# Performance work log

Hardware: AMD Instinct MI355X
Metric: run time of the kernel (lower is better)

## Reference

```python
import math
import jax, jax.numpy as jnp
import numpy as np

B, S, D_MODEL = 4, 2048, 512
H, D_KV = 8, 64
NUM_BUCKETS = 32
MAX_DISTANCE = 128  # T5 default


def _relative_position_bucket(rel_pos, bidirectional=True, num_buckets=NUM_BUCKETS, max_distance=MAX_DISTANCE):
    # Standard T5 bucketing (encoder: bidirectional=True since is_decoder=False).
    ret = jnp.zeros_like(rel_pos)
    if bidirectional:
        num_buckets //= 2
        ret = (rel_pos > 0).astype(jnp.int32) * num_buckets
        rel_pos = jnp.abs(rel_pos)
    else:
        rel_pos = -jnp.minimum(rel_pos, 0)
    max_exact = num_buckets // 2
    is_small = rel_pos < max_exact
    safe_rp = jnp.maximum(rel_pos, 1)  # avoid log(0); masked out by is_small
    val_if_large = max_exact + (
        jnp.log(safe_rp.astype(jnp.float32) / max_exact)
        / math.log(max_distance / max_exact)
        * (num_buckets - max_exact)
    ).astype(jnp.int32)
    val_if_large = jnp.minimum(val_if_large, num_buckets - 1)
    return ret + jnp.where(is_small, rel_pos, val_if_large)


def setup_inputs() -> dict:
    key = jax.random.key(0)
    ks = jax.random.split(key, 8)
    query = jax.random.normal(ks[0], (B, S, D_MODEL), dtype=jnp.float32)
    kk = jax.random.normal(ks[1], (B, S, D_MODEL), dtype=jnp.float32)
    vv = jax.random.normal(ks[2], (B, S, D_MODEL), dtype=jnp.float32)
    key_mask = jnp.ones((B, S), dtype=jnp.float32)
    scale = 1.0 / math.sqrt(D_MODEL)
    Wq = jax.random.normal(ks[3], (D_MODEL, H * D_KV), dtype=jnp.float32) * scale
    Wk = jax.random.normal(ks[4], (D_MODEL, H * D_KV), dtype=jnp.float32) * scale
    Wv = jax.random.normal(ks[5], (D_MODEL, H * D_KV), dtype=jnp.float32) * scale
    rel_emb = jax.random.normal(ks[6], (NUM_BUCKETS, H), dtype=jnp.float32) * 0.1
    return {"query": query, "key": kk, "value": vv, "key_mask": key_mask,
            "Wq": Wq, "Wk": Wk, "Wv": Wv, "rel_emb": rel_emb, "start_pos": 0}


def reference(query, key, value, key_mask, Wq, Wk, Wv, rel_emb, start_pos):
    Bq, Q, _ = query.shape
    K = key.shape[1]
    # projections (training path: no cache; equals start_pos=0 prefill)
    q = (query @ Wq).reshape(Bq, Q, H, D_KV)  # [B,Q,H,d]
    k = (key @ Wk).reshape(Bq, K, H, D_KV)
    v = (value @ Wv).reshape(Bq, K, H, D_KV)
    # T5: no 1/sqrt(d) scaling
    scores = jnp.einsum("bqhd,bkhd->bhqk", q, k)  # [B,H,Q,K]
    # relative position bias over [K,K], sliced to last Q rows
    ctx = jnp.arange(K)[:, None]
    mem = jnp.arange(K)[None, :]
    buckets = _relative_position_bucket(mem - ctx)  # [K,K]
    bias = rel_emb[buckets]  # [K,K,H]
    bias = jnp.transpose(bias, (2, 0, 1))[None, :, -Q:, :]  # [1,H,Q,K]
    scores = scores + bias
    # additive key mask
    add_mask = (1.0 - key_mask)[:, None, None, :] * -10000.0
    scores = scores + add_mask
    probs = jax.nn.softmax(scores, axis=-1)
    context = jnp.einsum("bhqk,bkhd->bqhd", probs, v)
    return context.reshape(Bq, Q, H * D_KV)
```

## Files before the change

kernel.cpp:

```cpp
#include <hip/hip_runtime.h>
#include <hip/hip_bf16.h>

typedef __attribute__((ext_vector_type(8))) _Float16 half8;
typedef __attribute__((ext_vector_type(2))) __fp16 fp16x2;
typedef __attribute__((ext_vector_type(4))) float f32x4;

#define LOG2E 1.4426950408889634f

__global__ __launch_bounds__(256) void cvt_h_kernel(const float* __restrict__ q,
                                                    const float* __restrict__ k,
                                                    const float* __restrict__ v,
                                                    _Float16* __restrict__ xq,
                                                    _Float16* __restrict__ xk,
                                                    _Float16* __restrict__ xv) {
  const int z = blockIdx.y;
  const float* x = z == 0 ? q : z == 1 ? k : v;
  _Float16* y = z == 0 ? xq : z == 1 ? xk : xv;
  size_t i = (size_t)blockIdx.x * 256 + threadIdx.x;
  const f32x4* p = (const f32x4*)x + i * 2;
  f32x4 a = p[0], b = p[1];
  half8 o;
  o[0] = (_Float16)a[0]; o[1] = (_Float16)a[1];
  o[2] = (_Float16)a[2]; o[3] = (_Float16)a[3];
  o[4] = (_Float16)b[0]; o[5] = (_Float16)b[1];
  o[6] = (_Float16)b[2]; o[7] = (_Float16)b[3];
  ((half8*)y)[i] = o;
}

__global__ __launch_bounds__(256) void wtrans_kernel(const float* __restrict__ Wq,
                                                     const float* __restrict__ Wk,
                                                     const float* __restrict__ Wv,
                                                     _Float16* __restrict__ wtq,
                                                     _Float16* __restrict__ wtk,
                                                     _Float16* __restrict__ wtv) {
  const int z = blockIdx.z;
  const float* W = z == 0 ? Wq : z == 1 ? Wk : Wv;
  _Float16* Wt = z == 0 ? wtq : z == 1 ? wtk : wtv;
  __shared__ float tile[32][33];
  int k0 = blockIdx.x * 32, n0 = blockIdx.y * 32;
  int c = threadIdx.x & 31, r0 = threadIdx.x >> 5;
  #pragma unroll
  for (int rr = 0; rr < 32; rr += 8)
    tile[r0 + rr][c] = W[(size_t)(k0 + r0 + rr) * 512 + n0 + c];
  __syncthreads();
  #pragma unroll
  for (int rr = 0; rr < 32; rr += 8)
    Wt[(size_t)(n0 + r0 + rr) * 512 + k0 + c] = (_Float16)tile[c][r0 + rr];
}

__global__ __launch_bounds__(256) void proj_kernel(const _Float16* __restrict__ Xq,
                                                   const _Float16* __restrict__ Xk,
                                                   const _Float16* __restrict__ Xv,
                                                   const _Float16* __restrict__ Wtq,
                                                   const _Float16* __restrict__ Wtk,
                                                   const _Float16* __restrict__ Wtv,
                                                   _Float16* __restrict__ Qp,
                                                   _Float16* __restrict__ Kp,
                                                   _Float16* __restrict__ Vt) {
  const int z = blockIdx.z;
  const _Float16* X  = z == 0 ? Xq : z == 1 ? Xk : Xv;
  const _Float16* Wt = z == 0 ? Wtq : z == 1 ? Wtk : Wtv;
  _Float16* outp     = z == 0 ? Qp : z == 1 ? Kp : Vt;

  __shared__ __align__(16) char lt_all[4 * 64 * 144];
  const int wave = threadIdx.x >> 6, lane = threadIdx.x & 63;
  const int g = lane >> 4, li = lane & 15;
  const int m0 = blockIdx.x * 128 + wave * 32;
  const int h = blockIdx.y;

  f32x4 acc[2][4];
  #pragma unroll
  for (int i = 0; i < 2; ++i)
    #pragma unroll
    for (int j = 0; j < 4; ++j) acc[i][j] = (f32x4){0.f, 0.f, 0.f, 0.f};

  const _Float16* xa = X + (size_t)m0 * 512;
  const _Float16* wb = Wt + (size_t)(h << 6) * 512;

  for (int k0 = 0; k0 < 512; k0 += 32) {
    half8 a[2], bw[4];
    #pragma unroll
    for (int rt = 0; rt < 2; ++rt)
      a[rt] = *(const half8*)(xa + (size_t)(rt * 16 + li) * 512 + k0 + g * 8);
    #pragma unroll
    for (int ct = 0; ct < 4; ++ct)
      bw[ct] = *(const half8*)(wb + (size_t)(ct * 16 + li) * 512 + k0 + g * 8);
    #pragma unroll
    for (int rt = 0; rt < 2; ++rt)
      #pragma unroll
      for (int ct = 0; ct < 4; ++ct)
        acc[rt][ct] = __builtin_amdgcn_mfma_f32_16x16x32_f16(a[rt], bw[ct], acc[rt][ct], 0, 0, 0);
  }

  const float qs = (z == 0) ? LOG2E : 1.0f;
  const int bidx = m0 >> 11, sbase = m0 & 2047;
  if (z != 2) {
    #pragma unroll
    for (int rt = 0; rt < 2; ++rt)
      #pragma unroll
      for (int r = 0; r < 4; ++r) {
        int s = sbase + rt * 16 + g * 4 + r;
        _Float16* orow = outp + ((size_t)((bidx * 8 + h) * 2048 + s) << 6);
        #pragma unroll
        for (int ct = 0; ct < 4; ++ct)
          orow[ct * 16 + li] = (_Float16)(acc[rt][ct][r] * qs);
      }
  } else {
    char* lt = lt_all + wave * (64 * 144);
    #pragma unroll
    for (int rt = 0; rt < 2; ++rt)
      #pragma unroll
      for (int ct = 0; ct < 4; ++ct)
        #pragma unroll
        for (int r = 0; r < 4; ++r) {
          int d = ct * 16 + li, sl = rt * 16 + g * 4 + r;
          *(_Float16*)(lt + d * 144 + ((sl * 2) ^ ((d & 7) << 4))) = (_Float16)acc[rt][ct][r];
        }
    __syncthreads();
    int d = lane;
    _Float16* vrow = outp + (size_t)((bidx * 8 + h) * 64 + d) * 2048 + sbase;
    #pragma unroll
    for (int c = 0; c < 4; ++c) {
      half8 vv = *(half8*)(lt + d * 144 + ((c * 16) ^ ((d & 7) << 4)));
      *(half8*)(vrow + c * 8) = vv;
    }
  }
}

__global__ __launch_bounds__(64, 2) void attn_kernel(const _Float16* __restrict__ Qp,
                                                     const _Float16* __restrict__ Kp,
                                                     const _Float16* __restrict__ Vt,
                                                     const float* __restrict__ kmask,
                                                     const float* __restrict__ rel_emb,
                                                     float* __restrict__ outp) {
  __shared__ float bias_tab[256];
  __shared__ __align__(16) char pb[2 * 2048];
  const int fid = blockIdx.x;
  const int nid = (fid & 7) * 256 + (fid >> 3);
  const int qt = nid & 63, bh = nid >> 6;
  const int b = bh >> 3, h = bh & 7;
  const int lane = threadIdx.x;
  const int g = lane >> 4, li = lane & 15;
  const int qw = qt * 32;

  for (int idx = lane; idx < 256; idx += 64) {
    int rel = idx - 128;
    int ret = rel > 0 ? 16 : 0;
    int rp = rel < 0 ? -rel : rel;
    int bb;
    if (rp < 8) bb = rp;
    else {
      int t = (rp >= 12) + (rp >= 16) + (rp >= 23) + (rp >= 32) +
              (rp >= 46) + (rp >= 64) + (rp >= 91);
      bb = 8 + t;
    }
    bias_tab[idx] = rel_emb[(ret + bb) * 8 + h] * LOG2E;
  }
  const float far_neg = rel_emb[15 * 8 + h] * LOG2E;
  const float far_pos = rel_emb[31 * 8 + h] * LOG2E;
  const float MASKC = 10000.0f * LOG2E;

  const _Float16* Qb = Qp + (size_t)bh * (2048 * 64);
  const _Float16* Kb = Kp + (size_t)bh * (2048 * 64);
  const _Float16* Vb = Vt + (size_t)bh * (64 * 2048);
  const float* mkb = kmask + b * 2048;

  half8 qa[2][2];
  #pragma unroll
  for (int s = 0; s < 2; ++s)
    #pragma unroll
    for (int kc = 0; kc < 2; ++kc)
      qa[s][kc] = *(const half8*)(Qb + (size_t)(qw + s * 16 + li) * 64 + kc * 32 + g * 8);

  f32x4 o[2][4];
  float m[2], l[2];
  #pragma unroll
  for (int s = 0; s < 2; ++s) {
    #pragma unroll
    for (int ct = 0; ct < 4; ++ct) o[s][ct] = (f32x4){0.f, 0.f, 0.f, 0.f};
    m[s] = -1e30f; l[s] = 0.f;
  }

  const int swz = (li & 7) << 4;
  half8 kA[4][2], kB[4][2];

  #pragma unroll
  for (int jt = 0; jt < 4; ++jt)
    #pragma unroll
    for (int kc = 0; kc < 2; ++kc)
      kA[jt][kc] = *(const half8*)(Kb + (size_t)(jt * 16 + li) * 64 + kc * 32 + g * 8);

  __syncthreads();

#define PREFETCH(DST, JN)                                                        \
  {                                                                              \
    int jn_ = (JN) < 2048 ? (JN) : 0;                                            \
    _Pragma("unroll")                                                            \
    for (int jt = 0; jt < 4; ++jt)                                               \
      _Pragma("unroll")                                                          \
      for (int kc = 0; kc < 2; ++kc)                                             \
        DST[jt][kc] = *(const half8*)(Kb + (size_t)(jn_ + jt * 16 + li) * 64 +   \
                                      kc * 32 + g * 8);                          \
  }

#define PROCESS(KB, J0)                                                          \
  {                                                                              \
    const int jb = (J0);            \
    f32x4 sc[2][4];                                                              \
    _Pragma("unroll")                                                            \
    for (int s = 0; s < 2; ++s)                                                  \
      _Pragma("unroll")                                                          \
      for (int jt = 0; jt < 4; ++jt) {                                           \
        f32x4 zz = (f32x4){0.f, 0.f, 0.f, 0.f};                                  \
        zz = __builtin_amdgcn_mfma_f32_16x16x32_f16(KB[jt][0], qa[s][0], zz, 0, 0, 0); \
        sc[s][jt] = __builtin_amdgcn_mfma_f32_16x16x32_f16(KB[jt][1], qa[s][1], zz, 0, 0, 0); \
      }                                                                          \
    _Pragma("unroll")                                                            \
    for (int jt = 0; jt < 4; ++jt) {                                             \
      int jlo = jb + jt * 16;                                                    \
      f32x4 m4 = *(const f32x4*)(mkb + jlo + 4 * g);                             \
      _Pragma("unroll")                                                          \
      for (int s = 0; s < 2; ++s) {                                              \
        int qlo = qw + s * 16;                                                   \
        if (jlo - (qlo + 15) >= 91) {                                            \
          _Pragma("unroll")                                                      \
          for (int r = 0; r < 4; ++r)                                            \
            sc[s][jt][r] += far_pos + (m4[r] - 1.0f) * MASKC;                    \
        } else if (jlo + 15 - qlo <= -91) {                                      \
          _Pragma("unroll")                                                      \
          for (int r = 0; r < 4; ++r)                                            \
            sc[s][jt][r] += far_neg + (m4[r] - 1.0f) * MASKC;                    \
        } else {                                                                 \
          int base = jlo + 4 * g - qlo - li + 128;                               \
          _Pragma("unroll")                                                      \
          for (int r = 0; r < 4; ++r)                                            \
            sc[s][jt][r] += bias_tab[base + r] + (m4[r] - 1.0f) * MASKC;         \
        }                                                                        \
      }                                                                          \
    }                                                                            \
    _Pragma("unroll")                                                            \
    for (int s = 0; s < 2; ++s) {                                                \
      float t = sc[s][0][0];                                                     \
      _Pragma("unroll")                                                          \
      for (int jt = 0; jt < 4; ++jt)                                             \
        _Pragma("unroll")                                                        \
        for (int r = 0; r < 4; ++r) t = fmaxf(t, sc[s][jt][r]);                  \
      t = fmaxf(t, __shfl_xor(t, 16));                                           \
      t = fmaxf(t, __shfl_xor(t, 32));                                           \
      float mnew = fmaxf(m[s], t);                                               \
      float scal = exp2f(m[s] - mnew);                                           \
      m[s] = mnew;                                                               \
      l[s] *= scal;                                                              \
      _Pragma("unroll")                                                          \
      for (int ct = 0; ct < 4; ++ct) o[s][ct] *= scal;                           \
      _Pragma("unroll")                                                          \
      for (int jt = 0; jt < 4; ++jt) {                                           \
        float p0 = exp2f(sc[s][jt][0] - m[s]), p1 = exp2f(sc[s][jt][1] - m[s]);  \
        float p2 = exp2f(sc[s][jt][2] - m[s]), p3 = exp2f(sc[s][jt][3] - m[s]);  \
        l[s] += (p0 + p1) + (p2 + p3);                                           \
        fp16x2 h01 = __builtin_amdgcn_cvt_pkrtz(p0, p1);                         \
        fp16x2 h23 = __builtin_amdgcn_cvt_pkrtz(p2, p3);                         \
        uint2 w;                                                                 \
        w.x = __builtin_bit_cast(unsigned, h01);                                 \
        w.y = __builtin_bit_cast(unsigned, h23);                                 \
        *(uint2*)(pb + s * 2048 + li * 128 + ((32 * jt + 8 * g) ^ swz)) = w;     \
      }                                                                          \
    }                                                                            \
    half8 pa[2][2];                                                              \
    _Pragma("unroll")                                                            \
    for (int s = 0; s < 2; ++s) {                                                \
      pa[s][0] = *(half8*)(pb + s * 2048 + li * 128 + ((16 * g) ^ swz));         \
      pa[s][1] = *(half8*)(pb + s * 2048 + li * 128 + ((64 + 16 * g) ^ swz));    \
    }                                                                            \
    __builtin_amdgcn_s_setprio(1);                                               \
    _Pragma("unroll")                                                            \
    for (int dct = 0; dct < 4; ++dct) {                                          \
      half8 vb0 = *(const half8*)(Vb + (size_t)(dct * 16 + li) * 2048 + jb + g * 8);      \
      half8 vb1 = *(const half8*)(Vb + (size_t)(dct * 16 + li) * 2048 + jb + 32 + g * 8); \
      _Pragma("unroll")                                                          \
      for (int s = 0; s < 2; ++s) {                                              \
        o[s][dct] = __builtin_amdgcn_mfma_f32_16x16x32_f16(vb0, pa[s][0], o[s][dct], 0, 0, 0); \
        o[s][dct] = __builtin_amdgcn_mfma_f32_16x16x32_f16(vb1, pa[s][1], o[s][dct], 0, 0, 0); \
      }                                                                          \
    }                                                                            \
    __builtin_amdgcn_s_setprio(0);                                               \
  }

  for (int j0 = 0; j0 < 2048; j0 += 128) {
    PREFETCH(kB, j0 + 64)
    PROCESS(kA, j0)
    PREFETCH(kA, j0 + 128)
    PROCESS(kB, j0 + 64)
  }
#undef PREFETCH
#undef PROCESS

  #pragma unroll
  for (int s = 0; s < 2; ++s) {
    float lf = l[s];
    lf += __shfl_xor(lf, 16);
    lf += __shfl_xor(lf, 32);
    float inv = 1.0f / lf;
    float* orow = outp + ((size_t)b * 2048 + qw + s * 16 + li) * 512 + h * 64;
    #pragma unroll
    for (int dct = 0; dct < 4; ++dct) {
      f32x4 ov = o[s][dct];
      ov[0] *= inv; ov[1] *= inv; ov[2] *= inv; ov[3] *= inv;
      *(f32x4*)(orow + dct * 16 + 4 * g) = ov;
    }
  }
}

extern "C" void kernel_launch(void* const* d_in, const int* in_sizes, int n_in,
                              void* d_out, int out_size, void* d_ws, size_t ws_size,
                              hipStream_t stream) {
  const float* query = (const float*)d_in[0];
  const float* key   = (const float*)d_in[1];
  const float* value = (const float*)d_in[2];
  const float* kmask = (const float*)d_in[3];
  const float* Wq    = (const float*)d_in[4];
  const float* Wk    = (const float*)d_in[5];
  const float* Wv    = (const float*)d_in[6];
  const float* rel   = (const float*)d_in[7];

  char* ws = (char*)d_ws;
  const size_t SZB = 8192ull * 512 * 2;
  const size_t WB  = 512ull * 512 * 2;
  _Float16* xq  = (_Float16*)(ws);
  _Float16* xk  = (_Float16*)(ws + SZB);
  _Float16* xv  = (_Float16*)(ws + 2 * SZB);
  _Float16* wtq = (_Float16*)(ws + 3 * SZB);
  _Float16* wtk = (_Float16*)(ws + 3 * SZB + WB);
  _Float16* wtv = (_Float16*)(ws + 3 * SZB + 2 * WB);
  _Float16* qp  = (_Float16*)(ws + 3 * SZB + 3 * WB);
  _Float16* kp  = (_Float16*)(ws + 4 * SZB + 3 * WB);
  _Float16* vt  = (_Float16*)(ws + 5 * SZB + 3 * WB);

  cvt_h_kernel<<<dim3(2048, 3), dim3(256), 0, stream>>>(query, key, value, xq, xk, xv);
  wtrans_kernel<<<dim3(16, 16, 3), dim3(256), 0, stream>>>(Wq, Wk, Wv, wtq, wtk, wtv);
  proj_kernel<<<dim3(64, 8, 3), dim3(256), 0, stream>>>(xq, xk, xv, wtq, wtk, wtv, qp, kp, vt);
  attn_kernel<<<dim3(2048), dim3(64), 0, stream>>>(qp, kp, vt, kmask, rel, (float*)d_out);
}
```

Before: 326.6 us.

## Split attention key range across two waves with LDS softmax merge

The attention block now uses two waves per 32-query tile. Each wave processes alternating 64-key chunks, and at the end the two partial (max, sum, output) states are merged through shared memory, flash-decoding style. This doubles the waves in flight and halves the serial key loop per wave, aiming to hide latency better. The cost is extra LDS, a barrier and a merge step, and the per-block resource use may limit occupancy. The mask term is also hoisted out of the inner s loop.

```diff
diff --git a/kernel.cpp b/kernel.cpp
--- a/kernel.cpp
+++ b/kernel.cpp
@@ -127,23 +127,24 @@
   }
 }
 
-__global__ __launch_bounds__(64, 2) void attn_kernel(const _Float16* __restrict__ Qp,
-                                                     const _Float16* __restrict__ Kp,
-                                                     const _Float16* __restrict__ Vt,
-                                                     const float* __restrict__ kmask,
-                                                     const float* __restrict__ rel_emb,
-                                                     float* __restrict__ outp) {
+__global__ __launch_bounds__(128, 4) void attn_kernel(const _Float16* __restrict__ Qp,
+                                                      const _Float16* __restrict__ Kp,
+                                                      const _Float16* __restrict__ Vt,
+                                                      const float* __restrict__ kmask,
+                                                      const float* __restrict__ rel_emb,
+                                                      float* __restrict__ outp) {
   __shared__ float bias_tab[256];
-  __shared__ __align__(16) char pb[2 * 2048];
+  __shared__ __align__(16) char pb_all[2 * 4096];
+  __shared__ __align__(16) f32x4 mrg[64][9];
   const int fid = blockIdx.x;
   const int nid = (fid & 7) * 256 + (fid >> 3);
   const int qt = nid & 63, bh = nid >> 6;
   const int b = bh >> 3, h = bh & 7;
-  const int lane = threadIdx.x;
+  const int wave = threadIdx.x >> 6, lane = threadIdx.x & 63;
   const int g = lane >> 4, li = lane & 15;
   const int qw = qt * 32;
 
-  for (int idx = lane; idx < 256; idx += 64) {
+  for (int idx = (int)threadIdx.x; idx < 256; idx += 128) {
     int rel = idx - 128;
     int ret = rel > 0 ? 16 : 0;
     int rp = rel < 0 ? -rel : rel;
@@ -182,13 +183,14 @@
   }
 
   const int swz = (li & 7) << 4;
+  char* pb = pb_all + wave * 4096;
   half8 kA[4][2], kB[4][2];
 
   #pragma unroll
   for (int jt = 0; jt < 4; ++jt)
     #pragma unroll
     for (int kc = 0; kc < 2; ++kc)
-      kA[jt][kc] = *(const half8*)(Kb + (size_t)(jt * 16 + li) * 64 + kc * 32 + g * 8);
+      kA[jt][kc] = *(const half8*)(Kb + (size_t)(wave * 64 + jt * 16 + li) * 64 + kc * 32 + g * 8);
 
   __syncthreads();
 
@@ -219,22 +221,25 @@
     for (int jt = 0; jt < 4; ++jt) {                                             \
       int jlo = jb + jt * 16;                                                    \
       f32x4 m4 = *(const f32x4*)(mkb + jlo + 4 * g);                             \
+      float mt[4];                                                               \
+      _Pragma("unroll")                                                          \
+      for (int r = 0; r < 4; ++r) mt[r] = (m4[r] - 1.0f) * MASKC;                \
       _Pragma("unroll")                                                          \
       for (int s = 0; s < 2; ++s) {                                              \
         int qlo = qw + s * 16;                                                   \
         if (jlo - (qlo + 15) >= 91) {                                            \
           _Pragma("unroll")                                                      \
           for (int r = 0; r < 4; ++r)                                            \
-            sc[s][jt][r] += far_pos + (m4[r] - 1.0f) * MASKC;                    \
+            sc[s][jt][r] += far_pos + mt[r];                                     \
         } else if (jlo + 15 - qlo <= -91) {                                      \
           _Pragma("unroll")                                                      \
           for (int r = 0; r < 4; ++r)                                            \
-            sc[s][jt][r] += far_neg + (m4[r] - 1.0f) * MASKC;                    \
+            sc[s][jt][r] += far_neg + mt[r];                                     \
         } else {                                                                 \
           int base = jlo + 4 * g - qlo - li + 128;                               \
           _Pragma("unroll")                                                      \
           for (int r = 0; r < 4; ++r)                                            \
-            sc[s][jt][r] += bias_tab[base + r] + (m4[r] - 1.0f) * MASKC;         \
+            sc[s][jt][r] += bias_tab[base + r] + mt[r];                          \
         }                                                                        \
       }                                                                          \
     }                                                                            \
@@ -286,27 +291,52 @@
     __builtin_amdgcn_s_setprio(0);                                               \
   }
 
-  for (int j0 = 0; j0 < 2048; j0 += 128) {
-    PREFETCH(kB, j0 + 64)
+  for (int j0 = wave * 64; j0 < 2048; j0 += 256) {
+    PREFETCH(kB, j0 + 128)
     PROCESS(kA, j0)
-    PREFETCH(kA, j0 + 128)
-    PROCESS(kB, j0 + 64)
+    PREFETCH(kA, j0 + 256)
+    PROCESS(kB, j0 + 128)
   }
 #undef PREFETCH
 #undef PROCESS
 
+  float lf[2];
   #pragma unroll
   for (int s = 0; s < 2; ++s) {
-    float lf = l[s];
-    lf += __shfl_xor(lf, 16);
-    lf += __shfl_xor(lf, 32);
-    float inv = 1.0f / lf;
-    float* orow = outp + ((size_t)b * 2048 + qw + s * 16 + li) * 512 + h * 64;
-    #pragma unroll
-    for (int dct = 0; dct < 4; ++dct) {
-      f32x4 ov = o[s][dct];
-      ov[0] *= inv; ov[1] *= inv; ov[2] *= inv; ov[3] *= inv;
-      *(f32x4*)(orow + dct * 16 + 4 * g) = ov;
+    float t = l[s];
+    t += __shfl_xor(t, 16);
+    t += __shfl_xor(t, 32);
+    lf[s] = t;
+  }
+
+  if (wave == 1) {
+    mrg[lane][0] = (f32x4){m[0], m[1], lf[0], lf[1]};
+    #pragma unroll
+    for (int s = 0; s < 2; ++s)
+      #pragma unroll
+      for (int dct = 0; dct < 4; ++dct)
+        mrg[lane][1 + s * 4 + dct] = o[s][dct];
+  }
+  __syncthreads();
+  if (wave == 0) {
+    f32x4 mm = mrg[lane][0];
+    #pragma unroll
+    for (int s = 0; s < 2; ++s) {
+      float M = fmaxf(m[s], mm[s]);
+      float a0 = exp2f(m[s] - M), a1 = exp2f(mm[s] - M);
+      float inv = 1.0f / (lf[s] * a0 + mm[2 + s] * a1);
+      a0 *= inv; a1 *= inv;
+      float* orow = outp + ((size_t)b * 2048 + qw + s * 16 + li) * 512 + h * 64;
+      #pragma unroll
+      for (int dct = 0; dct < 4; ++dct) {
+        f32x4 o1 = mrg[lane][1 + s * 4 + dct];
+        f32x4 ov;
+        ov[0] = o[s][dct][0] * a0 + o1[0] * a1;
+        ov[1] = o[s][dct][1] * a0 + o1[1] * a1;
+        ov[2] = o[s][dct][2] * a0 + o1[2] * a1;
+        ov[3] = o[s][dct][3] * a0 + o1[3] * a1;
+        *(f32x4*)(orow + dct * 16 + 4 * g) = ov;
+      }
     }
   }
 }
@@ -339,5 +369,5 @@
   cvt_h_kernel<<<dim3(2048, 3), dim3(256), 0, stream>>>(query, key, value, xq, xk, xv);
   wtrans_kernel<<<dim3(16, 16, 3), dim3(256), 0, stream>>>(Wq, Wk, Wv, wtq, wtk, wtv);
   proj_kernel<<<dim3(64, 8, 3), dim3(256), 0, stream>>>(xq, xk, xv, wtq, wtk, wtv, qp, kp, vt);
-  attn_kernel<<<dim3(2048), dim3(64), 0, stream>>>(qp, kp, vt, kmask, rel, (float*)d_out);
-}
+  attn_kernel<<<dim3(2048), dim3(128), 0, stream>>>(qp, kp, vt, kmask, rel, (float*)d_out);
+}
```

Result: slower. 520.1 us (+59.2%).
